# Kernel optimization log

Measured on AMD Instinct MI355X. Metric: run time of the kernel, lower is better.

The kernel has to match this reference:

```python
import jax, jax.numpy as jnp
import numpy as np

N, M, D, K = 32768, 1024, 512, 4096  # frames, motion_dim, latent_dim, codebook size
COMMITMENT_COST = 0.25
BN_EPS = 1e-5


def setup_inputs() -> dict:
    key = jax.random.key(0)
    ks = jax.random.split(key, 4)
    return {
        "x": jax.random.normal(ks[0], (N, M), dtype=jnp.float32),
        "enc_w": jax.random.normal(ks[1], (D, M), dtype=jnp.float32) * (1.0 / np.sqrt(M)),
        "enc_b": jnp.zeros((D,), jnp.float32),
        "bn_gamma": jnp.ones((D,), jnp.float32),
        "bn_beta": jnp.zeros((D,), jnp.float32),
        "bn_mean": jnp.zeros((D,), jnp.float32),
        "bn_var": jnp.ones((D,), jnp.float32),
        # nn.Embedding init: uniform(-1/K, 1/K)
        "codebook": jax.random.uniform(ks[2], (K, D), dtype=jnp.float32, minval=-1.0 / K, maxval=1.0 / K),
        "dec_w": jax.random.normal(ks[3], (M, D), dtype=jnp.float32) * (1.0 / np.sqrt(D)),
        "dec_b": jnp.zeros((M,), jnp.float32),
    }


def reference(x, enc_w, enc_b, bn_gamma, bn_beta, bn_mean, bn_var, codebook, dec_w, dec_b):
    # Encoder linear: [N, M] -> [N, D]
    z = x @ enc_w.T + enc_b
    # BatchNorm1d (inference mode, running stats)
    z = (z - bn_mean) * jax.lax.rsqrt(bn_var + BN_EPS) * bn_gamma + bn_beta

    # VQ (VQ_Payam_EMA, eval): squared L2 distances via ||z||^2 + ||e||^2 - 2 z e^T
    # distances: [N, K]
    distances = (
        jnp.sum(z * z, axis=1, keepdims=True)
        + jnp.sum(codebook * codebook, axis=1)
        - 2.0 * (z @ codebook.T)
    )
    idx = jnp.argmin(distances, axis=1)                    # [N]
    encodings = jax.nn.one_hot(idx, K, dtype=z.dtype)      # [N, K] one-hot scatter
    quantized = codebook[idx]                              # gather == encodings @ codebook

    # commitment loss (EMA variant: only e_latent_loss, quantized detached)
    e_latent_loss = jnp.mean((jax.lax.stop_gradient(quantized) - z) ** 2)
    loss = COMMITMENT_COST * e_latent_loss

    # straight-through estimator
    quantized_st = z + jax.lax.stop_gradient(quantized - z)

    avg_probs = jnp.mean(encodings, axis=0)                # [K]
    perplexity = jnp.exp(-jnp.sum(avg_probs * jnp.log(avg_probs + 1e-10)))

    # Decoder linear: [N, D] -> [N, M]
    out = quantized_st @ dec_w.T + dec_b
    return out, loss, perplexity, encodings
```

## Files before the change

kernel.cpp:

```cpp
#include <hip/hip_runtime.h>
#include <math.h>
#include <float.h>

#define N_FR 32768
#define M_DIM 1024
#define D_DIM 512
#define K_CB 4096

static const long long OUT_ELEMS = (long long)N_FR * M_DIM;
static const long long LOSS_OFF  = OUT_ELEMS;
static const long long ENC_OFF   = OUT_ELEMS + 2;
static const long long Z_OFF     = ENC_OFF + 2;
static const long long DC_OFF    = Z_OFF  + (long long)N_FR * D_DIM;
static const long long XH_OFF    = DC_OFF + (long long)K_CB * M_DIM;
static const long long XL_OFF    = XH_OFF + (long long)N_FR * M_DIM / 2;
static const long long WH_OFF    = XL_OFF + (long long)N_FR * M_DIM / 2;
static const long long WL_OFF    = WH_OFF + (long long)D_DIM * M_DIM / 2;
static const long long CH_OFF    = WL_OFF + (long long)D_DIM * M_DIM / 2;
static const long long CL_OFF    = CH_OFF + (long long)K_CB * D_DIM / 2;
static const long long ZH_OFF    = CL_OFF + (long long)K_CB * D_DIM / 2;
static const long long ZL_OFF    = ZH_OFF + (long long)N_FR * D_DIM / 2;
static const long long PV_OFF    = ZL_OFF + (long long)N_FR * D_DIM / 2;
static const long long PI_OFF    = PV_OFF + 4LL * N_FR;
static const long long DWH_OFF   = PI_OFF + 4LL * N_FR;
static const long long DWL_OFF   = DWH_OFF + (long long)M_DIM * D_DIM / 2;
static const long long SN_OFF    = DWL_OFF + (long long)M_DIM * D_DIM / 2;
static const long long LP_OFF    = SN_OFF + (long long)N_FR;

typedef __attribute__((ext_vector_type(8))) short bf16x8;
typedef __attribute__((ext_vector_type(8))) unsigned short u16x8;
typedef __attribute__((ext_vector_type(4))) float f32x4;

__device__ __forceinline__ unsigned short f2bf(float f) {
    unsigned u = __float_as_uint(f);
    return (unsigned short)((u + 0x7fffu + ((u >> 16) & 1u)) >> 16);
}
__device__ __forceinline__ float bf2f(unsigned short h) {
    return __uint_as_float(((unsigned)h) << 16);
}
__device__ __forceinline__ void gl_lds16(const unsigned short* g, unsigned short* l) {
    __builtin_amdgcn_global_load_lds(
        (const __attribute__((address_space(1))) unsigned int*)g,
        (__attribute__((address_space(3))) unsigned int*)l,
        16, 0, 0);
}

__global__ __launch_bounds__(256)
void conv_split(const float* __restrict__ in, unsigned short* __restrict__ hi,
                unsigned short* __restrict__ lo, int C, int KC)
{
    int w = blockIdx.x * 4 + (threadIdx.x >> 6);
    int lane = threadIdx.x & 63;
    int bn = w / KC, ck = w % KC;
    int r = bn * 16 + (lane & 15);
    int c = ck * 32 + (lane >> 4) * 8;
    const float4* p = (const float4*)&in[(size_t)r * C + c];
    float4 v0 = p[0], v1 = p[1];
    float f[8] = {v0.x, v0.y, v0.z, v0.w, v1.x, v1.y, v1.z, v1.w};
    u16x8 hv, lv;
    #pragma unroll
    for (int j = 0; j < 8; ++j) {
        unsigned short h = f2bf(f[j]);
        hv[j] = h;
        lv[j] = f2bf(f[j] - bf2f(h));
    }
    size_t o = (size_t)w * 512 + lane * 8;
    *(u16x8*)&hi[o] = hv;
    *(u16x8*)&lo[o] = lv;
}

template<int EPI>
__global__ __launch_bounds__(256)
void gemm_pack(const unsigned short* __restrict__ ah_, const unsigned short* __restrict__ al_,
               const unsigned short* __restrict__ bh_, const unsigned short* __restrict__ bl_,
               const float* __restrict__ bias, const float* __restrict__ gamma,
               const float* __restrict__ beta, const float* __restrict__ mean,
               const float* __restrict__ var, float* __restrict__ C,
               int nbi, int nkb, int NJ)
{
    __shared__ unsigned short lds[16384];
    const int tid = threadIdx.x, wid = tid >> 6, lane = tid & 63;
    const int wr = wid >> 1, wc = wid & 1;
    const int bi = blockIdx.x % nbi, bj = blockIdx.x / nbi;

    f32x4 acc[4][4];
    #pragma unroll
    for (int i = 0; i < 4; ++i)
        #pragma unroll
        for (int j = 0; j < 4; ++j) acc[i][j] = (f32x4){0.f, 0.f, 0.f, 0.f};

    for (int ks = 0; ks < nkb; ++ks) {
        __syncthreads();
        #pragma unroll
        for (int q = 0; q < 8; ++q) {
            int id = wid * 8 + q;
            int arr = id >> 3, rb = id & 7;
            const unsigned short* base = arr == 0 ? ah_ : arr == 1 ? al_ : arr == 2 ? bh_ : bl_;
            size_t b = (size_t)((arr < 2 ? bi : bj) * 8 + rb) * nkb + ks;
            gl_lds16(base + b * 512 + lane * 8, lds + id * 512);
        }
        __syncthreads();
        bf16x8 ah[4], al[4], bh[4], bl[4];
        #pragma unroll
        for (int i = 0; i < 4; ++i) {
            ah[i] = *(const bf16x8*)(lds + (4 * wr + i) * 512 + lane * 8);
            al[i] = *(const bf16x8*)(lds + 4096 + (4 * wr + i) * 512 + lane * 8);
        }
        #pragma unroll
        for (int j = 0; j < 4; ++j) {
            bh[j] = *(const bf16x8*)(lds + 8192  + (4 * wc + j) * 512 + lane * 8);
            bl[j] = *(const bf16x8*)(lds + 12288 + (4 * wc + j) * 512 + lane * 8);
        }
        #pragma unroll
        for (int i = 0; i < 4; ++i)
            #pragma unroll
            for (int j = 0; j < 4; ++j) {
                acc[i][j] = __builtin_amdgcn_mfma_f32_16x16x32_bf16(ah[i], bh[j], acc[i][j], 0, 0, 0);
                acc[i][j] = __builtin_amdgcn_mfma_f32_16x16x32_bf16(ah[i], bl[j], acc[i][j], 0, 0, 0);
                acc[i][j] = __builtin_amdgcn_mfma_f32_16x16x32_bf16(al[i], bh[j], acc[i][j], 0, 0, 0);
            }
    }
    #pragma unroll
    for (int j = 0; j < 4; ++j) {
        int col = bj * 128 + wc * 64 + j * 16 + (lane & 15);
        float bvv = bias[col];
        float g = 0.f, bt = 0.f, mn = 0.f, rs = 0.f;
        if (EPI == 0) {
            g  = gamma[col];
            bt = beta[col];
            mn = mean[col];
            rs = (float)(1.0 / sqrt((double)var[col] + 1e-5));
        }
        #pragma unroll
        for (int i = 0; i < 4; ++i)
            #pragma unroll
            for (int r = 0; r < 4; ++r) {
                int row = bi * 128 + wr * 64 + i * 16 + (lane >> 4) * 4 + r;
                float v = acc[i][j][r] + bvv;
                if (EPI == 0) v = (v - mn) * rs * g + bt;
                C[(size_t)row * NJ + col] = v;
            }
    }
}

__global__ __launch_bounds__(256, 2)
void argmin_mfma(const unsigned short* __restrict__ zh, const unsigned short* __restrict__ zl,
                 const unsigned short* __restrict__ ch, const unsigned short* __restrict__ cl,
                 const float* __restrict__ se,
                 float* __restrict__ pval, int* __restrict__ pidx)
{
    __shared__ unsigned short lds[24576];
    __shared__ float sv[128][2];
    __shared__ int   si[128][2];
    const int tid = threadIdx.x, wid = tid >> 6, lane = tid & 63;
    const int wr = wid >> 1, wc = wid & 1;
    const int row0 = (int)(blockIdx.x >> 2) * 128;
    const int grp  = (int)(blockIdx.x & 3);

    float bv[16];
    int   bi[16];
    #pragma unroll
    for (int s = 0; s < 16; ++s) { bv[s] = FLT_MAX; bi[s] = 0x7fffffff; }

    for (int cc = 0; cc < 4; ++cc) {
        const int code0 = grp * 1024 + cc * 256;
        f32x4 acc[4][8];
        #pragma unroll
        for (int i = 0; i < 4; ++i)
            #pragma unroll
            for (int j = 0; j < 8; ++j) acc[i][j] = (f32x4){0.f, 0.f, 0.f, 0.f};

        for (int ks = 0; ks < 16; ++ks) {
            __syncthreads();
            #pragma unroll
            for (int q = 0; q < 12; ++q) {
                int id = wid * 12 + q;
                const unsigned short* src;
                if (id < 16) {
                    int a = id >> 3, rb = id & 7;
                    src = (a ? zl : zh) + ((size_t)((row0 >> 4) + rb) * 16 + ks) * 512 + lane * 8;
                } else {
                    int id2 = id - 16;
                    int a = id2 >> 4, cb2 = id2 & 15;
                    src = (a ? cl : ch) + ((size_t)((code0 >> 4) + cb2) * 16 + ks) * 512 + lane * 8;
                }
                gl_lds16(src, lds + id * 512);
            }
            __syncthreads();
            bf16x8 ah[4], al[4];
            #pragma unroll
            for (int i = 0; i < 4; ++i) {
                ah[i] = *(const bf16x8*)(lds + (wr * 4 + i) * 512 + lane * 8);
                al[i] = *(const bf16x8*)(lds + 4096 + (wr * 4 + i) * 512 + lane * 8);
            }
            #pragma unroll
            for (int j = 0; j < 8; ++j) {
                bf16x8 bhj = *(const bf16x8*)(lds + 8192  + (wc * 8 + j) * 512 + lane * 8);
                bf16x8 blj = *(const bf16x8*)(lds + 16384 + (wc * 8 + j) * 512 + lane * 8);
                #pragma unroll
                for (int i = 0; i < 4; ++i) {
                    acc[i][j] = __builtin_amdgcn_mfma_f32_16x16x32_bf16(ah[i], bhj, acc[i][j], 0, 0, 0);
                    acc[i][j] = __builtin_amdgcn_mfma_f32_16x16x32_bf16(ah[i], blj, acc[i][j], 0, 0, 0);
                    acc[i][j] = __builtin_amdgcn_mfma_f32_16x16x32_bf16(al[i], bhj, acc[i][j], 0, 0, 0);
                }
            }
        }
        #pragma unroll
        for (int j = 0; j < 8; ++j) {
            int code = code0 + wc * 128 + j * 16 + (lane & 15);
            float sev = se[code];
            #pragma unroll
            for (int i = 0; i < 4; ++i)
                #pragma unroll
                for (int r = 0; r < 4; ++r) {
                    float key = sev - 2.0f * acc[i][j][r];
                    int s = i * 4 + r;
                    if (key < bv[s]) { bv[s] = key; bi[s] = code; }
                }
        }
    }
    #pragma unroll
    for (int s = 0; s < 16; ++s) {
        #pragma unroll
        for (int off = 1; off < 16; off <<= 1) {
            float ov = __shfl_xor(bv[s], off);
            int   oi = __shfl_xor(bi[s], off);
            if (ov < bv[s] || (ov == bv[s] && oi < bi[s])) { bv[s] = ov; bi[s] = oi; }
        }
    }
    if ((lane & 15) == 0) {
        #pragma unroll
        for (int i = 0; i < 4; ++i)
            #pragma unroll
            for (int r = 0; r < 4; ++r) {
                int row = wr * 64 + i * 16 + (lane >> 4) * 4 + r;
                sv[row][wc] = bv[i * 4 + r];
                si[row][wc] = bi[i * 4 + r];
            }
    }
    __syncthreads();
    if (tid < 128) {
        float v0 = sv[tid][0], v1 = sv[tid][1];
        int   i0 = si[tid][0], i1 = si[tid][1];
        float bvv = v0; int bii = i0;
        if (v1 < v0 || (v1 == v0 && i1 < i0)) { bvv = v1; bii = i1; }
        pval[(size_t)grp * N_FR + row0 + tid] = bvv;
        pidx[(size_t)grp * N_FR + row0 + tid] = bii;
    }
}

__global__ __launch_bounds__(256)
void merge_k(const float* __restrict__ pval, const int* __restrict__ pidx,
             const float* __restrict__ sn,
             int* __restrict__ fidx, int* __restrict__ counts,
             float* __restrict__ lpart)
{
    __shared__ float ls[4];
    int tid = threadIdx.x;
    int n = blockIdx.x * 256 + tid;
    float best = pval[n];
    int   bi   = pidx[n];
    #pragma unroll
    for (int c = 1; c < 4; ++c) {
        float v = pval[(long long)c * N_FR + n];
        int   i = pidx[(long long)c * N_FR + n];
        if (v < best) { best = v; bi = i; }
    }
    fidx[n] = bi;
    atomicAdd(&counts[bi], 1);
    float rl = sn[n] + best;
    #pragma unroll
    for (int off = 32; off; off >>= 1) rl += __shfl_xor(rl, off);
    if ((tid & 63) == 0) ls[tid >> 6] = rl;
    __syncthreads();
    if (tid == 0) lpart[blockIdx.x] = ls[0] + ls[1] + ls[2] + ls[3];
}

__global__ __launch_bounds__(256)
void rownorm_k(const float* __restrict__ A, float* __restrict__ sn)
{
    int row  = blockIdx.x * 4 + (threadIdx.x >> 6);
    int lane = threadIdx.x & 63;
    const float4* p = (const float4*)(A + (long long)row * D_DIM + lane * 8);
    float4 a = p[0], b = p[1];
    float s = a.x*a.x + a.y*a.y + a.z*a.z + a.w*a.w
            + b.x*b.x + b.y*b.y + b.z*b.z + b.w*b.w;
    #pragma unroll
    for (int off = 32; off; off >>= 1) s += __shfl_xor(s, off);
    if (lane == 0) sn[row] = s;
}

__global__ __launch_bounds__(256)
void gather_k(const float* __restrict__ DC, const int* __restrict__ fidx,
              float* __restrict__ outp)
{
    int n = blockIdx.x;
    int id = fidx[n];
    float4 v = ((const float4*)(DC + (long long)id * M_DIM))[threadIdx.x];
    ((float4*)(outp + (long long)n * M_DIM))[threadIdx.x] = v;
}

__global__ __launch_bounds__(256)
void enc_write(const int* __restrict__ fidx, float* __restrict__ enc)
{
    int n    = blockIdx.x * 4 + (threadIdx.x >> 6);
    int lane = threadIdx.x & 63;
    int idx  = fidx[n];
    float4* row = (float4*)(enc + (size_t)n * K_CB);
    #pragma unroll
    for (int c = 0; c < 16; ++c) {
        int p = c * 64 + lane;
        int b4 = p * 4;
        float4 v;
        v.x = (idx == b4 + 0) ? 1.0f : 0.0f;
        v.y = (idx == b4 + 1) ? 1.0f : 0.0f;
        v.z = (idx == b4 + 2) ? 1.0f : 0.0f;
        v.w = (idx == b4 + 3) ? 1.0f : 0.0f;
        row[p] = v;
    }
}

__global__ __launch_bounds__(256)
void fin_k(const int* __restrict__ counts, const float* __restrict__ lpart,
           float* __restrict__ scal)
{
    __shared__ double sh[4], lh[4];
    int tid = threadIdx.x;
    double s = 0.0;
    for (int k = tid; k < K_CB; k += 256) {
        double p = (double)counts[k] / (double)N_FR;
        s += p * log(p + 1e-10);
    }
    double l = (tid < 128) ? (double)lpart[tid] : 0.0;
    #pragma unroll
    for (int off = 32; off; off >>= 1) {
        s += __shfl_xor(s, off);
        l += __shfl_xor(l, off);
    }
    if ((tid & 63) == 0) { sh[tid >> 6] = s; lh[tid >> 6] = l; }
    __syncthreads();
    if (tid == 0) {
        double tot = sh[0] + sh[1] + sh[2] + sh[3];
        double L   = lh[0] + lh[1] + lh[2] + lh[3];
        scal[0] = (float)(0.25 * L / ((double)N_FR * (double)D_DIM));
        scal[1] = (float)exp(-tot);
    }
}

extern "C" void kernel_launch(void* const* d_in, const int* in_sizes, int n_in,
                              void* d_out, int out_size, void* d_ws, size_t ws_size,
                              hipStream_t stream)
{
    (void)in_sizes; (void)n_in; (void)out_size; (void)ws_size;
    const float* x        = (const float*)d_in[0];
    const float* enc_w    = (const float*)d_in[1];
    const float* enc_b    = (const float*)d_in[2];
    const float* bn_gamma = (const float*)d_in[3];
    const float* bn_beta  = (const float*)d_in[4];
    const float* bn_mean  = (const float*)d_in[5];
    const float* bn_var   = (const float*)d_in[6];
    const float* cb       = (const float*)d_in[7];
    const float* dec_w    = (const float*)d_in[8];
    const float* dec_b    = (const float*)d_in[9];

    float* outp = (float*)d_out;
    float* z    = outp + Z_OFF;
    float* dc   = outp + DC_OFF;
    unsigned short* xh  = (unsigned short*)(outp + XH_OFF);
    unsigned short* xl  = (unsigned short*)(outp + XL_OFF);
    unsigned short* whp = (unsigned short*)(outp + WH_OFF);
    unsigned short* wlp = (unsigned short*)(outp + WL_OFF);
    unsigned short* chp = (unsigned short*)(outp + CH_OFF);
    unsigned short* clp = (unsigned short*)(outp + CL_OFF);
    unsigned short* zhp = (unsigned short*)(outp + ZH_OFF);
    unsigned short* zlp = (unsigned short*)(outp + ZL_OFF);
    float* pval = outp + PV_OFF;
    int*   pidx = (int*)(outp + PI_OFF);
    unsigned short* dwh = (unsigned short*)(outp + DWH_OFF);
    unsigned short* dwl = (unsigned short*)(outp + DWL_OFF);
    float* sn    = outp + SN_OFF;
    float* lpart = outp + LP_OFF;

    char*   wsb    = (char*)d_ws;
    int*    fidx   = (int*)wsb;
    int*    counts = (int*)(wsb + 131072);
    float*  se     = (float*)(wsb + 147456);

    hipMemsetAsync(counts, 0, 16384, stream);

    conv_split<<<dim3(16384), 256, 0, stream>>>(x, xh, xl, M_DIM, M_DIM / 32);
    conv_split<<<dim3(256),   256, 0, stream>>>(enc_w, whp, wlp, M_DIM, M_DIM / 32);
    conv_split<<<dim3(1024),  256, 0, stream>>>(cb, chp, clp, D_DIM, D_DIM / 32);
    conv_split<<<dim3(256),   256, 0, stream>>>(dec_w, dwh, dwl, D_DIM, D_DIM / 32);
    rownorm_k<<<dim3(K_CB / 4), 256, 0, stream>>>(cb, se);

    gemm_pack<0><<<dim3(1024), 256, 0, stream>>>(xh, xl, whp, wlp,
        enc_b, bn_gamma, bn_beta, bn_mean, bn_var, z, 256, 32, D_DIM);
    conv_split<<<dim3(8192), 256, 0, stream>>>(z, zhp, zlp, D_DIM, D_DIM / 32);
    rownorm_k<<<dim3(N_FR / 4), 256, 0, stream>>>(z, sn);

    gemm_pack<1><<<dim3(256), 256, 0, stream>>>(chp, clp, dwh, dwl,
        dec_b, nullptr, nullptr, nullptr, nullptr, dc, 32, 16, M_DIM);

    argmin_mfma<<<dim3(1024), 256, 0, stream>>>(zhp, zlp, chp, clp, se, pval, pidx);
    merge_k<<<dim3(N_FR / 256), 256, 0, stream>>>(pval, pidx, sn, fidx, counts, lpart);

    gather_k<<<dim3(N_FR), 256, 0, stream>>>(dc, fidx, outp);
    fin_k<<<dim3(1), 256, 0, stream>>>(counts, lpart, outp + LOSS_OFF);

    enc_write<<<dim3(N_FR / 4), 256, 0, stream>>>(fidx, outp + ENC_OFF);
}
```

Measured before the change: 758.4 us.

## Fuse encoder GEMM epilogue with bf16 split packing and row-norm partials

The encoder GEMM now applies BatchNorm, computes per-row squared-norm partials, and writes the hi/lo bf16 split of z directly in the packed tile layout through LDS. This removes the fp32 z round trip, the separate conv_split pass over z, and the rownorm kernel. merge_k sums eight partial norms instead of reading one. conv_split's lane-to-row mapping is also changed so that every packed tile matches the new layout.

```diff
diff --git a/kernel.cpp b/kernel.cpp
--- a/kernel.cpp
+++ b/kernel.cpp
@@ -10,22 +10,21 @@
 static const long long OUT_ELEMS = (long long)N_FR * M_DIM;
 static const long long LOSS_OFF  = OUT_ELEMS;
 static const long long ENC_OFF   = OUT_ELEMS + 2;
-static const long long Z_OFF     = ENC_OFF + 2;
-static const long long DC_OFF    = Z_OFF  + (long long)N_FR * D_DIM;
-static const long long XH_OFF    = DC_OFF + (long long)K_CB * M_DIM;
-static const long long XL_OFF    = XH_OFF + (long long)N_FR * M_DIM / 2;
-static const long long WH_OFF    = XL_OFF + (long long)N_FR * M_DIM / 2;
-static const long long WL_OFF    = WH_OFF + (long long)D_DIM * M_DIM / 2;
-static const long long CH_OFF    = WL_OFF + (long long)D_DIM * M_DIM / 2;
-static const long long CL_OFF    = CH_OFF + (long long)K_CB * D_DIM / 2;
-static const long long ZH_OFF    = CL_OFF + (long long)K_CB * D_DIM / 2;
-static const long long ZL_OFF    = ZH_OFF + (long long)N_FR * D_DIM / 2;
-static const long long PV_OFF    = ZL_OFF + (long long)N_FR * D_DIM / 2;
-static const long long PI_OFF    = PV_OFF + 4LL * N_FR;
-static const long long DWH_OFF   = PI_OFF + 4LL * N_FR;
-static const long long DWL_OFF   = DWH_OFF + (long long)M_DIM * D_DIM / 2;
-static const long long SN_OFF    = DWL_OFF + (long long)M_DIM * D_DIM / 2;
-static const long long LP_OFF    = SN_OFF + (long long)N_FR;
+static const long long DC_OFF  = ENC_OFF + 2;
+static const long long XH_OFF  = DC_OFF  + (long long)K_CB * M_DIM;
+static const long long XL_OFF  = XH_OFF  + (long long)N_FR * M_DIM / 2;
+static const long long WH_OFF  = XL_OFF  + (long long)N_FR * M_DIM / 2;
+static const long long WL_OFF  = WH_OFF  + (long long)D_DIM * M_DIM / 2;
+static const long long CH_OFF  = WL_OFF  + (long long)D_DIM * M_DIM / 2;
+static const long long CL_OFF  = CH_OFF  + (long long)K_CB * D_DIM / 2;
+static const long long ZH_OFF  = CL_OFF  + (long long)K_CB * D_DIM / 2;
+static const long long ZL_OFF  = ZH_OFF  + (long long)N_FR * D_DIM / 2;
+static const long long PV_OFF  = ZL_OFF  + (long long)N_FR * D_DIM / 2;
+static const long long PI_OFF  = PV_OFF  + 4LL * N_FR;
+static const long long DWH_OFF = PI_OFF  + 4LL * N_FR;
+static const long long DWL_OFF = DWH_OFF + (long long)M_DIM * D_DIM / 2;
+static const long long SNP_OFF = DWL_OFF + (long long)M_DIM * D_DIM / 2;
+static const long long LP_OFF  = SNP_OFF + 8LL * N_FR;
 
 typedef __attribute__((ext_vector_type(8))) short bf16x8;
 typedef __attribute__((ext_vector_type(8))) unsigned short u16x8;
@@ -52,8 +51,9 @@
     int w = blockIdx.x * 4 + (threadIdx.x >> 6);
     int lane = threadIdx.x & 63;
     int bn = w / KC, ck = w % KC;
-    int r = bn * 16 + (lane & 15);
-    int c = ck * 32 + (lane >> 4) * 8;
+    int rho = lane >> 2, omg = lane & 3;
+    int r = bn * 16 + rho;
+    int c = ck * 32 + omg * 8;
     const float4* p = (const float4*)&in[(size_t)r * C + c];
     float4 v0 = p[0], v1 = p[1];
     float f[8] = {v0.x, v0.y, v0.z, v0.w, v1.x, v1.y, v1.z, v1.w};
@@ -64,18 +64,127 @@
         hv[j] = h;
         lv[j] = f2bf(f[j] - bf2f(h));
     }
-    size_t o = (size_t)w * 512 + lane * 8;
+    size_t o = (size_t)w * 512 + (size_t)(rho + 16 * omg) * 8;
     *(u16x8*)&hi[o] = hv;
     *(u16x8*)&lo[o] = lv;
 }
 
-template<int EPI>
+__global__ __launch_bounds__(256)
+void enc_fused(const unsigned short* __restrict__ xh_, const unsigned short* __restrict__ xl_,
+               const unsigned short* __restrict__ wh_, const unsigned short* __restrict__ wl_,
+               const float* __restrict__ bias, const float* __restrict__ gamma,
+               const float* __restrict__ beta, const float* __restrict__ mean,
+               const float* __restrict__ var,
+               unsigned short* __restrict__ zh, unsigned short* __restrict__ zl,
+               float* __restrict__ snp)
+{
+    __shared__ unsigned short lds[16384];
+    const int tid = threadIdx.x, wid = tid >> 6, lane = tid & 63;
+    const int wr = wid >> 1, wc = wid & 1;
+    const int bi = blockIdx.x & 255, bj = blockIdx.x >> 8;
+
+    f32x4 acc[4][4];
+    #pragma unroll
+    for (int i = 0; i < 4; ++i)
+        #pragma unroll
+        for (int j = 0; j < 4; ++j) acc[i][j] = (f32x4){0.f, 0.f, 0.f, 0.f};
+
+    for (int ks = 0; ks < 32; ++ks) {
+        __syncthreads();
+        #pragma unroll
+        for (int q = 0; q < 8; ++q) {
+            int id = wid * 8 + q;
+            int arr = id >> 3, rb = id & 7;
+            const unsigned short* base = arr == 0 ? xh_ : arr == 1 ? xl_ : arr == 2 ? wh_ : wl_;
+            size_t b = (size_t)((arr < 2 ? bi : bj) * 8 + rb) * 32 + ks;
+            gl_lds16(base + b * 512 + lane * 8, lds + id * 512);
+        }
+        __syncthreads();
+        bf16x8 ah[4], al[4], bh[4], bl[4];
+        #pragma unroll
+        for (int i = 0; i < 4; ++i) {
+            ah[i] = *(const bf16x8*)(lds + (4 * wr + i) * 512 + lane * 8);
+            al[i] = *(const bf16x8*)(lds + 4096 + (4 * wr + i) * 512 + lane * 8);
+        }
+        #pragma unroll
+        for (int j = 0; j < 4; ++j) {
+            bh[j] = *(const bf16x8*)(lds + 8192  + (4 * wc + j) * 512 + lane * 8);
+            bl[j] = *(const bf16x8*)(lds + 12288 + (4 * wc + j) * 512 + lane * 8);
+        }
+        #pragma unroll
+        for (int i = 0; i < 4; ++i)
+            #pragma unroll
+            for (int j = 0; j < 4; ++j) {
+                acc[i][j] = __builtin_amdgcn_mfma_f32_16x16x32_bf16(ah[i], bh[j], acc[i][j], 0, 0, 0);
+                acc[i][j] = __builtin_amdgcn_mfma_f32_16x16x32_bf16(ah[i], bl[j], acc[i][j], 0, 0, 0);
+                acc[i][j] = __builtin_amdgcn_mfma_f32_16x16x32_bf16(al[i], bh[j], acc[i][j], 0, 0, 0);
+            }
+    }
+
+    #pragma unroll
+    for (int j = 0; j < 4; ++j) {
+        int col = bj * 128 + wc * 64 + j * 16 + (lane & 15);
+        float bvv = bias[col], g = gamma[col], bt = beta[col], mn = mean[col];
+        float rs = (float)(1.0 / sqrt((double)var[col] + 1e-5));
+        #pragma unroll
+        for (int i = 0; i < 4; ++i)
+            #pragma unroll
+            for (int r = 0; r < 4; ++r) {
+                float v = acc[i][j][r] + bvv;
+                acc[i][j][r] = (v - mn) * rs * g + bt;
+            }
+    }
+
+    #pragma unroll
+    for (int i = 0; i < 4; ++i)
+        #pragma unroll
+        for (int r = 0; r < 4; ++r) {
+            float s = 0.f;
+            #pragma unroll
+            for (int j = 0; j < 4; ++j) s = fmaf(acc[i][j][r], acc[i][j][r], s);
+            #pragma unroll
+            for (int off = 1; off < 16; off <<= 1) s += __shfl_xor(s, off);
+            if ((lane & 15) == 0) {
+                int row = bi * 128 + wr * 64 + i * 16 + (lane >> 4) * 4 + r;
+                snp[(size_t)(bj * 2 + wc) * N_FR + row] = s;
+            }
+        }
+
+    __syncthreads();
+    #pragma unroll
+    for (int half = 0; half < 2; ++half) {
+        #pragma unroll
+        for (int i = 0; i < 4; ++i)
+            #pragma unroll
+            for (int j = 0; j < 4; ++j)
+                #pragma unroll
+                for (int r = 0; r < 4; ++r) {
+                    int rl = wr * 64 + i * 16 + (lane >> 4) * 4 + r;
+                    int cl = wc * 64 + j * 16 + (lane & 15);
+                    float v = acc[i][j][r];
+                    unsigned short h = f2bf(v);
+                    unsigned short out = half == 0 ? h : f2bf(v - bf2f(h));
+                    int lblk = (rl >> 4) * 4 + (cl >> 5);
+                    lds[lblk * 512 + ((rl & 15) + 16 * ((cl >> 3) & 3)) * 8 + (cl & 7)] = out;
+                }
+        __syncthreads();
+        unsigned short* dst = half == 0 ? zh : zl;
+        #pragma unroll
+        for (int q = 0; q < 8; ++q) {
+            int s = q * 256 + tid;
+            u16x8 val = *(const u16x8*)(lds + (size_t)s * 8);
+            int lblk = s >> 6, l = s & 63;
+            size_t b = (size_t)(bi * 8 + (lblk >> 2)) * 16 + (bj * 4 + (lblk & 3));
+            *(u16x8*)(dst + b * 512 + l * 8) = val;
+        }
+        __syncthreads();
+    }
+}
+
 __global__ __launch_bounds__(256)
 void gemm_pack(const unsigned short* __restrict__ ah_, const unsigned short* __restrict__ al_,
                const unsigned short* __restrict__ bh_, const unsigned short* __restrict__ bl_,
-               const float* __restrict__ bias, const float* __restrict__ gamma,
-               const float* __restrict__ beta, const float* __restrict__ mean,
-               const float* __restrict__ var, float* __restrict__ C,
+               const float* __restrict__ bias, float* __restrict__ C,
                int nbi, int nkb, int NJ)
 {
     __shared__ unsigned short lds[16384];
@@ -124,21 +233,12 @@
     for (int j = 0; j < 4; ++j) {
         int col = bj * 128 + wc * 64 + j * 16 + (lane & 15);
         float bvv = bias[col];
-        float g = 0.f, bt = 0.f, mn = 0.f, rs = 0.f;
-        if (EPI == 0) {
-            g  = gamma[col];
-            bt = beta[col];
-            mn = mean[col];
-            rs = (float)(1.0 / sqrt((double)var[col] + 1e-5));
-        }
         #pragma unroll
         for (int i = 0; i < 4; ++i)
             #pragma unroll
             for (int r = 0; r < 4; ++r) {
                 int row = bi * 128 + wr * 64 + i * 16 + (lane >> 4) * 4 + r;
-                float v = acc[i][j][r] + bvv;
-                if (EPI == 0) v = (v - mn) * rs * g + bt;
-                C[(size_t)row * NJ + col] = v;
+                C[(size_t)row * NJ + col] = acc[i][j][r] + bvv;
             }
     }
 }
@@ -251,7 +351,7 @@
 
 __global__ __launch_bounds__(256)
 void merge_k(const float* __restrict__ pval, const int* __restrict__ pidx,
-             const float* __restrict__ sn,
+             const float* __restrict__ snp,
              int* __restrict__ fidx, int* __restrict__ counts,
              float* __restrict__ lpart)
 {
@@ -268,7 +368,10 @@
     }
     fidx[n] = bi;
     atomicAdd(&counts[bi], 1);
-    float rl = sn[n] + best;
+    float sn = 0.f;
+    #pragma unroll
+    for (int c = 0; c < 8; ++c) sn += snp[(long long)c * N_FR + n];
+    float rl = sn + best;
     #pragma unroll
     for (int off = 32; off; off >>= 1) rl += __shfl_xor(rl, off);
     if ((tid & 63) == 0) ls[tid >> 6] = rl;
@@ -364,7 +467,6 @@
     const float* dec_b    = (const float*)d_in[9];
 
     float* outp = (float*)d_out;
-    float* z    = outp + Z_OFF;
     float* dc   = outp + DC_OFF;
     unsigned short* xh  = (unsigned short*)(outp + XH_OFF);
     unsigned short* xl  = (unsigned short*)(outp + XL_OFF);
@@ -378,7 +480,7 @@
     int*   pidx = (int*)(outp + PI_OFF);
     unsigned short* dwh = (unsigned short*)(outp + DWH_OFF);
     unsigned short* dwl = (unsigned short*)(outp + DWL_OFF);
-    float* sn    = outp + SN_OFF;
+    float* snp   = outp + SNP_OFF;
     float* lpart = outp + LP_OFF;
 
     char*   wsb    = (char*)d_ws;
@@ -394,16 +496,13 @@
     conv_split<<<dim3(256),   256, 0, stream>>>(dec_w, dwh, dwl, D_DIM, D_DIM / 32);
     rownorm_k<<<dim3(K_CB / 4), 256, 0, stream>>>(cb, se);
 
-    gemm_pack<0><<<dim3(1024), 256, 0, stream>>>(xh, xl, whp, wlp,
-        enc_b, bn_gamma, bn_beta, bn_mean, bn_var, z, 256, 32, D_DIM);
-    conv_split<<<dim3(8192), 256, 0, stream>>>(z, zhp, zlp, D_DIM, D_DIM / 32);
-    rownorm_k<<<dim3(N_FR / 4), 256, 0, stream>>>(z, sn);
-
-    gemm_pack<1><<<dim3(256), 256, 0, stream>>>(chp, clp, dwh, dwl,
-        dec_b, nullptr, nullptr, nullptr, nullptr, dc, 32, 16, M_DIM);
+    enc_fused<<<dim3(1024), 256, 0, stream>>>(xh, xl, whp, wlp,
+        enc_b, bn_gamma, bn_beta, bn_mean, bn_var, zhp, zlp, snp);
+
+    gemm_pack<<<dim3(256), 256, 0, stream>>>(chp, clp, dwh, dwl, dec_b, dc, 32, 16, M_DIM);
 
     argmin_mfma<<<dim3(1024), 256, 0, stream>>>(zhp, zlp, chp, clp, se, pval, pidx);
-    merge_k<<<dim3(N_FR / 256), 256, 0, stream>>>(pval, pidx, sn, fidx, counts, lpart);
+    merge_k<<<dim3(N_FR / 256), 256, 0, stream>>>(pval, pidx, snp, fidx, counts, lpart);
 
     gather_k<<<dim3(N_FR), 256, 0, stream>>>(dc, fidx, outp);
     fin_k<<<dim3(1), 256, 0, stream>>>(counts, lpart, outp + LOSS_OFF);
```

New measurement: 804.8 us. 6.1% more time.

## Double-buffer argmin LDS staging, drop codebook low part, fuse conversion kernels

Applied to the files above, without the earlier changes.

The argmin kernel now flattens its code-chunk and k-step loops into one loop. It double-buffers LDS so the next tile's global-to-LDS loads overlap the current MFMAs, with one barrier per step. It also drops the codebook low-bf16 term, cutting MFMAs per step from three to two and shrinking staged data, at some precision cost that could flip near-tie argmins. The four bf16 split-conversion launches are merged into a single kernel to cut launch overhead.

```diff
diff --git a/kernel.cpp b/kernel.cpp
--- a/kernel.cpp
+++ b/kernel.cpp
@@ -45,11 +45,9 @@
         16, 0, 0);
 }
 
-__global__ __launch_bounds__(256)
-void conv_split(const float* __restrict__ in, unsigned short* __restrict__ hi,
-                unsigned short* __restrict__ lo, int C, int KC)
-{
-    int w = blockIdx.x * 4 + (threadIdx.x >> 6);
+__device__ __forceinline__ void conv_body(const float* in, unsigned short* hi,
+                                          unsigned short* lo, int C, int KC, int w)
+{
     int lane = threadIdx.x & 63;
     int bn = w / KC, ck = w % KC;
     int r = bn * 16 + (lane & 15);
@@ -67,6 +65,31 @@
     size_t o = (size_t)w * 512 + lane * 8;
     *(u16x8*)&hi[o] = hv;
     *(u16x8*)&lo[o] = lv;
+}
+
+__global__ __launch_bounds__(256)
+void conv_all(const float* __restrict__ x,  const float* __restrict__ ew,
+              const float* __restrict__ cb, const float* __restrict__ dw,
+              unsigned short* __restrict__ xh,  unsigned short* __restrict__ xl,
+              unsigned short* __restrict__ wh,  unsigned short* __restrict__ wl,
+              unsigned short* __restrict__ ch,  unsigned short* __restrict__ cl,
+              unsigned short* __restrict__ dwh, unsigned short* __restrict__ dwl)
+{
+    int b = blockIdx.x;
+    const float* in; unsigned short* hi; unsigned short* lo; int C; int w0;
+    if (b < 16384)      { in = x;  hi = xh;  lo = xl;  C = 1024; w0 = b; }
+    else if (b < 16640) { in = ew; hi = wh;  lo = wl;  C = 1024; w0 = b - 16384; }
+    else if (b < 17664) { in = cb; hi = ch;  lo = cl;  C = 512;  w0 = b - 16640; }
+    else                { in = dw; hi = dwh; lo = dwl; C = 512;  w0 = b - 17664; }
+    int KC = C / 32;
+    conv_body(in, hi, lo, C, KC, w0 * 4 + (threadIdx.x >> 6));
+}
+
+__global__ __launch_bounds__(256)
+void conv_split(const float* __restrict__ in, unsigned short* __restrict__ hi,
+                unsigned short* __restrict__ lo, int C, int KC)
+{
+    conv_body(in, hi, lo, C, KC, blockIdx.x * 4 + (threadIdx.x >> 6));
 }
 
 template<int EPI>
@@ -145,11 +168,11 @@
 
 __global__ __launch_bounds__(256, 2)
 void argmin_mfma(const unsigned short* __restrict__ zh, const unsigned short* __restrict__ zl,
-                 const unsigned short* __restrict__ ch, const unsigned short* __restrict__ cl,
+                 const unsigned short* __restrict__ ch,
                  const float* __restrict__ se,
                  float* __restrict__ pval, int* __restrict__ pidx)
 {
-    __shared__ unsigned short lds[24576];
+    __shared__ unsigned short lds[32768];
     __shared__ float sv[128][2];
     __shared__ int   si[128][2];
     const int tid = threadIdx.x, wid = tid >> 6, lane = tid & 63;
@@ -157,68 +180,78 @@
     const int row0 = (int)(blockIdx.x >> 2) * 128;
     const int grp  = (int)(blockIdx.x & 3);
 
+    auto stage = [&](int t, int bufsel) {
+        int cc = t >> 4, ks = t & 15;
+        int code0 = grp * 1024 + cc * 256;
+        unsigned short* dst = lds + bufsel * 16384;
+        #pragma unroll
+        for (int q = 0; q < 8; ++q) {
+            int id = wid * 8 + q;
+            const unsigned short* src;
+            if (id < 16) {
+                int a = id >> 3, rb = id & 7;
+                src = (a ? zl : zh) + ((size_t)((row0 >> 4) + rb) * 16 + ks) * 512 + lane * 8;
+            } else {
+                int cb2 = id - 16;
+                src = ch + ((size_t)((code0 >> 4) + cb2) * 16 + ks) * 512 + lane * 8;
+            }
+            gl_lds16(src, dst + id * 512);
+        }
+    };
+
     float bv[16];
     int   bi[16];
     #pragma unroll
     for (int s = 0; s < 16; ++s) { bv[s] = FLT_MAX; bi[s] = 0x7fffffff; }
 
-    for (int cc = 0; cc < 4; ++cc) {
-        const int code0 = grp * 1024 + cc * 256;
-        f32x4 acc[4][8];
-        #pragma unroll
-        for (int i = 0; i < 4; ++i)
-            #pragma unroll
-            for (int j = 0; j < 8; ++j) acc[i][j] = (f32x4){0.f, 0.f, 0.f, 0.f};
-
-        for (int ks = 0; ks < 16; ++ks) {
-            __syncthreads();
-            #pragma unroll
-            for (int q = 0; q < 12; ++q) {
-                int id = wid * 12 + q;
-                const unsigned short* src;
-                if (id < 16) {
-                    int a = id >> 3, rb = id & 7;
-                    src = (a ? zl : zh) + ((size_t)((row0 >> 4) + rb) * 16 + ks) * 512 + lane * 8;
-                } else {
-                    int id2 = id - 16;
-                    int a = id2 >> 4, cb2 = id2 & 15;
-                    src = (a ? cl : ch) + ((size_t)((code0 >> 4) + cb2) * 16 + ks) * 512 + lane * 8;
-                }
-                gl_lds16(src, lds + id * 512);
-            }
-            __syncthreads();
-            bf16x8 ah[4], al[4];
+    f32x4 acc[4][8];
+    #pragma unroll
+    for (int i = 0; i < 4; ++i)
+        #pragma unroll
+        for (int j = 0; j < 8; ++j) acc[i][j] = (f32x4){0.f, 0.f, 0.f, 0.f};
+
+    stage(0, 0);
+    __syncthreads();
+
+    for (int t = 0; t < 64; ++t) {
+        int cur = t & 1;
+        if (t < 63) stage(t + 1, cur ^ 1);
+        const unsigned short* L = lds + cur * 16384;
+        bf16x8 ah[4], al[4];
+        #pragma unroll
+        for (int i = 0; i < 4; ++i) {
+            ah[i] = *(const bf16x8*)(L + (wr * 4 + i) * 512 + lane * 8);
+            al[i] = *(const bf16x8*)(L + 4096 + (wr * 4 + i) * 512 + lane * 8);
+        }
+        #pragma unroll
+        for (int j = 0; j < 8; ++j) {
+            bf16x8 bhj = *(const bf16x8*)(L + 8192 + (wc * 8 + j) * 512 + lane * 8);
             #pragma unroll
             for (int i = 0; i < 4; ++i) {
-                ah[i] = *(const bf16x8*)(lds + (wr * 4 + i) * 512 + lane * 8);
-                al[i] = *(const bf16x8*)(lds + 4096 + (wr * 4 + i) * 512 + lane * 8);
-            }
+                acc[i][j] = __builtin_amdgcn_mfma_f32_16x16x32_bf16(ah[i], bhj, acc[i][j], 0, 0, 0);
+                acc[i][j] = __builtin_amdgcn_mfma_f32_16x16x32_bf16(al[i], bhj, acc[i][j], 0, 0, 0);
+            }
+        }
+        if ((t & 15) == 15) {
+            int code0 = grp * 1024 + (t >> 4) * 256;
             #pragma unroll
             for (int j = 0; j < 8; ++j) {
-                bf16x8 bhj = *(const bf16x8*)(lds + 8192  + (wc * 8 + j) * 512 + lane * 8);
-                bf16x8 blj = *(const bf16x8*)(lds + 16384 + (wc * 8 + j) * 512 + lane * 8);
+                int code = code0 + wc * 128 + j * 16 + (lane & 15);
+                float sev = se[code];
                 #pragma unroll
-                for (int i = 0; i < 4; ++i) {
-                    acc[i][j] = __builtin_amdgcn_mfma_f32_16x16x32_bf16(ah[i], bhj, acc[i][j], 0, 0, 0);
-                    acc[i][j] = __builtin_amdgcn_mfma_f32_16x16x32_bf16(ah[i], blj, acc[i][j], 0, 0, 0);
-                    acc[i][j] = __builtin_amdgcn_mfma_f32_16x16x32_bf16(al[i], bhj, acc[i][j], 0, 0, 0);
-                }
-            }
-        }
-        #pragma unroll
-        for (int j = 0; j < 8; ++j) {
-            int code = code0 + wc * 128 + j * 16 + (lane & 15);
-            float sev = se[code];
-            #pragma unroll
-            for (int i = 0; i < 4; ++i)
-                #pragma unroll
-                for (int r = 0; r < 4; ++r) {
-                    float key = sev - 2.0f * acc[i][j][r];
-                    int s = i * 4 + r;
-                    if (key < bv[s]) { bv[s] = key; bi[s] = code; }
-                }
-        }
-    }
+                for (int i = 0; i < 4; ++i)
+                    #pragma unroll
+                    for (int r = 0; r < 4; ++r) {
+                        float key = sev - 2.0f * acc[i][j][r];
+                        int s = i * 4 + r;
+                        if (key < bv[s]) { bv[s] = key; bi[s] = code; }
+                        acc[i][j][r] = 0.f;
+                    }
+            }
+        }
+        __syncthreads();
+    }
+
     #pragma unroll
     for (int s = 0; s < 16; ++s) {
         #pragma unroll
@@ -388,10 +421,8 @@
 
     hipMemsetAsync(counts, 0, 16384, stream);
 
-    conv_split<<<dim3(16384), 256, 0, stream>>>(x, xh, xl, M_DIM, M_DIM / 32);
-    conv_split<<<dim3(256),   256, 0, stream>>>(enc_w, whp, wlp, M_DIM, M_DIM / 32);
-    conv_split<<<dim3(1024),  256, 0, stream>>>(cb, chp, clp, D_DIM, D_DIM / 32);
-    conv_split<<<dim3(256),   256, 0, stream>>>(dec_w, dwh, dwl, D_DIM, D_DIM / 32);
+    conv_all<<<dim3(17920), 256, 0, stream>>>(x, enc_w, cb, dec_w,
+        xh, xl, whp, wlp, chp, clp, dwh, dwl);
     rownorm_k<<<dim3(K_CB / 4), 256, 0, stream>>>(cb, se);
 
     gemm_pack<0><<<dim3(1024), 256, 0, stream>>>(xh, xl, whp, wlp,
@@ -402,7 +433,7 @@
     gemm_pack<1><<<dim3(256), 256, 0, stream>>>(chp, clp, dwh, dwl,
         dec_b, nullptr, nullptr, nullptr, nullptr, dc, 32, 16, M_DIM);
 
-    argmin_mfma<<<dim3(1024), 256, 0, stream>>>(zhp, zlp, chp, clp, se, pval, pidx);
+    argmin_mfma<<<dim3(1024), 256, 0, stream>>>(zhp, zlp, chp, se, pval, pidx);
     merge_k<<<dim3(N_FR / 256), 256, 0, stream>>>(pval, pidx, sn, fidx, counts, lpart);
 
     gather_k<<<dim3(N_FR), 256, 0, stream>>>(dc, fidx, outp);
```

After: 662.2 us. 12.7% less time.
